# Kernel optimization log

Hardware: AMD Instinct MI355X
Metric: run time of the kernel (lower is better)

The kernel has to match this reference:

```python
import jax, jax.numpy as jnp
import numpy as np

B, S, E = 4, 2048, 768
DFF = 4 * E
EPS = 1e-5


def _layernorm(x, g, b):
    mu = jnp.mean(x, axis=-1, keepdims=True)
    var = jnp.mean(jnp.square(x - mu), axis=-1, keepdims=True)
    return (x - mu) * jax.lax.rsqrt(var + EPS) * g + b


def setup_inputs() -> dict:
    key = jax.random.key(0)
    ks = jax.random.split(key, 16)
    w = lambda k, shp: jax.random.normal(k, shp, dtype=jnp.float32) * 0.02
    inp = {
        "x": jax.random.normal(ks[0], (B, S, E), dtype=jnp.float32),
        "kv": jax.random.normal(ks[1], (B, S, E), dtype=jnp.float32),
        "wq_w": w(ks[2], (E, E)), "wq_b": jnp.zeros((E,), jnp.float32),
        "wk_w": w(ks[3], (E, E)), "wk_b": jnp.zeros((E,), jnp.float32),
        "wv_w": w(ks[4], (E, E)), "wv_b": jnp.zeros((E,), jnp.float32),
        "ln1_g": jnp.ones((E,), jnp.float32), "ln1_b": jnp.zeros((E,), jnp.float32),
        "wq2_w": w(ks[5], (E, E)), "wq2_b": jnp.zeros((E,), jnp.float32),
        "wk2_w": w(ks[6], (E, E)), "wk2_b": jnp.zeros((E,), jnp.float32),
        "wv2_w": w(ks[7], (E, E)), "wv2_b": jnp.zeros((E,), jnp.float32),
        "ln2_g": jnp.ones((E,), jnp.float32), "ln2_b": jnp.zeros((E,), jnp.float32),
        "w1": w(ks[8], (DFF, E)), "b1": jnp.zeros((DFF,), jnp.float32),
        "w2": w(ks[9], (E, DFF)), "b2": jnp.zeros((E,), jnp.float32),
        "ln3_g": jnp.ones((E,), jnp.float32), "ln3_b": jnp.zeros((E,), jnp.float32),
    }
    return inp


def reference(x, kv, wq_w, wq_b, wk_w, wk_b, wv_w, wv_b, ln1_g, ln1_b,
              wq2_w, wq2_b, wk2_w, wk2_b, wv2_w, wv2_b, ln2_g, ln2_b,
              w1, b1, w2, b2, ln3_g, ln3_b):
    scalar = 1.0 / np.sqrt(E).astype(np.float32)
    mask_value = jnp.finfo(x.dtype).min
    s = x.shape[1]
    causal = jnp.triu(jnp.ones((s, s), dtype=bool), k=1)  # True above diagonal -> masked

    # ---- causal self-attention (single head, full E) ----
    q = x @ wq_w.T + wq_b
    k = x @ wk_w.T + wk_b
    v = x @ wv_w.T + wv_b
    scores = jnp.einsum('bqe,bke->bqk', q, k) * scalar
    scores = jnp.where(causal, mask_value, scores)
    h1 = jnp.einsum('bqk,bke->bqe', jax.nn.softmax(scores, axis=-1), v)
    x = _layernorm(x + h1, ln1_g, ln1_b)

    # ---- cross-attention over kv (no mask) ----
    q2 = x @ wq2_w.T + wq2_b
    k2 = kv @ wk2_w.T + wk2_b
    v2 = kv @ wv2_w.T + wv2_b
    scores2 = jnp.einsum('bqe,bke->bqk', q2, k2) * scalar
    h2 = jnp.einsum('bqk,bke->bqe', jax.nn.softmax(scores2, axis=-1), v2)
    x = _layernorm(x + h2, ln2_g, ln2_b)

    # ---- MLP: Linear -> ReLU -> Linear -> ReLU (note trailing ReLU) ----
    h = jax.nn.relu(x @ w1.T + b1)
    mlp = jax.nn.relu(h @ w2.T + b2)
    return _layernorm(x + mlp, ln3_g, ln3_b)
```

## Files before the change

### kernel.cpp

```cpp
#include <hip/hip_runtime.h>
#include <hip/hip_bf16.h>
#include <math.h>


typedef __bf16 bf16_t;
typedef bf16_t bf16x8 __attribute__((ext_vector_type(8)));
typedef float f32x4 __attribute__((ext_vector_type(4)));

#define TBM 128
#define TBN 128
#define TBK 32
#define CPAD 136

struct MMDesc {
    const bf16_t* A;
    const bf16_t* B;
    const float* bias;
    __hip_bfloat16* C;
    float* lsum;
    int koff;
    int trans;
};
struct MMArgs { MMDesc g[8]; };

__device__ __forceinline__ void load16(const bf16_t* g, bf16_t* l) {
    __builtin_amdgcn_global_load_lds(
        (const __attribute__((address_space(1))) unsigned int*)g,
        (__attribute__((address_space(3))) unsigned int*)l, 16, 0, 0);
}

__device__ __forceinline__ void mm_core(
    const bf16_t* Ag, const bf16_t* Bg, int lda, int ldb, int K,
    bf16_t* Asm, bf16_t* Bsm, int w, int l, int wm, int wn, f32x4 acc[4][4]) {
    const int fr = l & 15;
    const int kq = (l >> 4) * 8;
    const long rsA = (long)64 * lda, rsB = (long)64 * ldb;
    bf16_t* Al = Asm + w * 512;
    bf16_t* Bl = Bsm + w * 512;

    for (int k0 = 0; k0 < K; k0 += 64) {
        load16(Ag + k0, Al);
        load16(Ag + rsA + k0, Al + 2048);
        load16(Bg + k0, Bl);
        load16(Bg + rsB + k0, Bl + 2048);
        load16(Ag + k0 + 32, Al + 4096);
        load16(Ag + rsA + k0 + 32, Al + 6144);
        load16(Bg + k0 + 32, Bl + 4096);
        load16(Bg + rsB + k0 + 32, Bl + 6144);
        __syncthreads();

#pragma unroll
        for (int t = 0; t < 2; ++t) {
            const bf16_t* As = Asm + t * 4096;
            const bf16_t* Bs = Bsm + t * 4096;
            bf16x8 af[4], bfr[4];
#pragma unroll
            for (int i = 0; i < 4; ++i)
                af[i] = *(const bf16x8*)(As + (wm + i * 16 + fr) * TBK + kq);
#pragma unroll
            for (int j = 0; j < 4; ++j)
                bfr[j] = *(const bf16x8*)(Bs + (wn + j * 16 + fr) * TBK + kq);
#pragma unroll
            for (int i = 0; i < 4; ++i)
#pragma unroll
                for (int j = 0; j < 4; ++j)
                    acc[i][j] = __builtin_amdgcn_mfma_f32_16x16x32_bf16(
                        af[i], bfr[j], acc[i][j], 0, 0, 0);
        }
        __syncthreads();
    }
}

__device__ __forceinline__ void tile_out(
    const __hip_bfloat16* ct, __hip_bfloat16* base, long ldc, int tid) {
#pragma unroll
    for (int u = 0; u < 8; ++u) {
        const int e = u * 2048 + tid * 8;
        const int rl = e >> 7, cl = e & 127;
        *(uint4*)(base + (long)rl * ldc + cl) = *(const uint4*)(ct + rl * CPAD + cl);
    }
}

template <bool RELU, bool CLAMPK>
__global__ __launch_bounds__(256) void mm_std(
    MMArgs args, int M, int N, int K, int lda, int ldb, float scale, int GX) {
    __shared__ __align__(16) bf16_t smem[128 * CPAD];
    bf16_t* Asm = smem;
    bf16_t* Bsm = smem + 8192;

    const MMDesc dsc = args.g[blockIdx.z];

    const int lin = blockIdx.x;
    const int panel = lin / (8 * GX);
    const int rem = lin - panel * 8 * GX;
    const int bx = rem >> 3;
    const int by = panel * 8 + (rem & 7);

    const int m0 = by * TBM, n0 = bx * TBN;
    const int tid = threadIdx.x, w = tid >> 6, l = tid & 63;
    const int wm = (w >> 1) * 64, wn = (w & 1) * 64;
    const int srow = w * 16 + (l >> 2);
    const int scol = (l & 3) * 8;
    const int fr = l & 15;

    f32x4 acc[4][4];
    const f32x4 z4 = {0.f, 0.f, 0.f, 0.f};
#pragma unroll
    for (int i = 0; i < 4; ++i)
#pragma unroll
        for (int j = 0; j < 4; ++j) acc[i][j] = z4;

    int Keff = K;
    if (CLAMPK) {
        int km = (by + 1) * TBM - dsc.koff;
        Keff = km < K ? km : K;
    }
    if (!CLAMPK || Keff > 0)
        mm_core(dsc.A + (long)(m0 + srow) * lda + scol,
                dsc.B + (long)(n0 + srow) * ldb + scol,
                lda, ldb, Keff, Asm, Bsm, w, l, wm, wn, acc);

    __hip_bfloat16* ct = (__hip_bfloat16*)smem;
    const int erow = (l >> 4) * 4;
#pragma unroll
    for (int j = 0; j < 4; ++j) {
        const int cl = wn + j * 16 + fr;
        const float bv = dsc.bias ? dsc.bias[n0 + cl] : 0.f;
#pragma unroll
        for (int i = 0; i < 4; ++i) {
            const int rl = wm + i * 16 + erow;
#pragma unroll
            for (int r = 0; r < 4; ++r) {
                float v = acc[i][j][r] * scale + bv;
                if (RELU) v = fmaxf(v, 0.f);
                const int idx = dsc.trans ? (cl * CPAD + rl + r) : ((rl + r) * CPAD + cl);
                ct[idx] = __float2bfloat16(v);
            }
        }
    }
    __syncthreads();
    __hip_bfloat16* base;
    long ldc;
    if (dsc.trans) {
        base = dsc.C + ((long)(m0 >> 11) * N + n0) * 2048 + (m0 & 2047);
        ldc = 2048;
    } else {
        base = dsc.C + (long)m0 * N + n0;
        ldc = N;
    }
    tile_out(ct, base, ldc, tid);
}

template <bool CAUSAL>
__global__ __launch_bounds__(256) void mm_exp(
    MMArgs args, int N, int K, int lda, int ldb, float scale, int GX) {
    __shared__ __align__(16) bf16_t smem[128 * CPAD];
    bf16_t* Asm = smem;
    bf16_t* Bsm = smem + 8192;

    const MMDesc dsc = args.g[blockIdx.z];

    int bx, by;
    if (CAUSAL) {
        const int t = blockIdx.x;
        by = (int)((sqrtf(8.f * t + 1.f) - 1.f) * 0.5f);
        while ((by + 1) * (by + 2) / 2 <= t) ++by;
        while (by * (by + 1) / 2 > t) --by;
        bx = t - by * (by + 1) / 2;
    } else {
        const int lin = blockIdx.x;
        const int panel = lin / (8 * GX);
        const int rem = lin - panel * 8 * GX;
        bx = rem >> 3;
        by = panel * 8 + (rem & 7);
    }

    const int m0 = by * TBM, n0 = bx * TBN;
    const int tid = threadIdx.x, w = tid >> 6, l = tid & 63;
    const int wm = (w >> 1) * 64, wn = (w & 1) * 64;
    const int srow = w * 16 + (l >> 2);
    const int scol = (l & 3) * 8;
    const int fr = l & 15;

    f32x4 acc[4][4];
    const f32x4 z4 = {0.f, 0.f, 0.f, 0.f};
#pragma unroll
    for (int i = 0; i < 4; ++i)
#pragma unroll
        for (int j = 0; j < 4; ++j) acc[i][j] = z4;

    mm_core(dsc.A + (long)(m0 + srow) * lda + scol,
            dsc.B + (long)(n0 + srow) * ldb + scol,
            lda, ldb, K, Asm, Bsm, w, l, wm, wn, acc);

    __hip_bfloat16* ct = (__hip_bfloat16*)smem;
    const int erow = (l >> 4) * 4;
#pragma unroll
    for (int i = 0; i < 4; ++i) {
#pragma unroll
        for (int r = 0; r < 4; ++r) {
            const int rl = wm + i * 16 + erow + r;
            const int grow = m0 + rl;
            float rs = 0.f;
#pragma unroll
            for (int j = 0; j < 4; ++j) {
                const int cl = wn + j * 16 + fr;
                float e;
                if (CAUSAL && (n0 + cl) > grow)
                    e = 0.f;
                else
                    e = __expf(acc[i][j][r] * scale);
                ct[rl * CPAD + cl] = __float2bfloat16(e);
                rs += e;
            }
#pragma unroll
            for (int o = 8; o > 0; o >>= 1) rs += __shfl_down(rs, o, 16);
            if ((l & 15) == 0) atomicAdd(&dsc.lsum[grow], rs);
        }
    }
    __syncthreads();
    tile_out(ct, dsc.C + (long)m0 * N + n0, N, tid);
}

__device__ __forceinline__ float waveReduceSum(float v) {
#pragma unroll
    for (int o = 32; o > 0; o >>= 1) v += __shfl_down(v, o, 64);
    return v;
}
__device__ __forceinline__ float blockReduceSum(float v, float* s) {
    int lane = threadIdx.x & 63, w = threadIdx.x >> 6;
    v = waveReduceSum(v);
    __syncthreads();
    if (lane == 0) s[w] = v;
    __syncthreads();
    return s[0] + s[1] + s[2] + s[3];
}

template <bool BR, bool XF32>
__global__ __launch_bounds__(256) void ln_kernel(
    const float* __restrict__ xf, const __hip_bfloat16* __restrict__ xh,
    const __hip_bfloat16* __restrict__ h1, const __hip_bfloat16* __restrict__ h2,
    const float* __restrict__ hbias, const float* __restrict__ lsum,
    const float* __restrict__ g, const float* __restrict__ beta,
    float* __restrict__ outf, __hip_bfloat16* __restrict__ outb) {
    __shared__ float red[4];
    const int E = 768;
    const long row = blockIdx.x;
    const float hscale = lsum ? (1.f / lsum[row]) : 1.f;

    float vals[3];
    float sum = 0.f;
#pragma unroll
    for (int i = 0; i < 3; ++i) {
        int c = threadIdx.x + i * 256;
        float t = __bfloat162float(h1[row * E + c]) + __bfloat162float(h2[row * E + c]);
        if (BR) t = fmaxf(t + hbias[c], 0.f);
        else t *= hscale;
        float xv = XF32 ? xf[row * E + c] : __bfloat162float(xh[row * E + c]);
        vals[i] = xv + t;
        sum += vals[i];
    }
    sum = blockReduceSum(sum, red);
    const float mean = sum * (1.f / 768.f);

    float ss = 0.f;
#pragma unroll
    for (int i = 0; i < 3; ++i) {
        float d = vals[i] - mean;
        ss += d * d;
    }
    ss = blockReduceSum(ss, red);
    const float inv = rsqrtf(ss * (1.f / 768.f) + 1e-5f);

#pragma unroll
    for (int i = 0; i < 3; ++i) {
        int c = threadIdx.x + i * 256;
        float v = (vals[i] - mean) * inv * g[c] + beta[c];
        if (outf) outf[row * E + c] = v;
        if (outb) outb[row * E + c] = __float2bfloat16(v);
    }
}

struct CvtPtrs {
    const float* s[10];
    __hip_bfloat16* d[10];
};
__global__ __launch_bounds__(256) void cvt_all(CvtPtrs p) {
    int bid = blockIdx.x, seg, off;
    if (bid < 3456) {
        seg = bid / 576;
        off = (bid % 576) * 1024;
    } else if (bid < 8064) {
        int t = bid - 3456;
        seg = 6 + t / 2304;
        off = (t % 2304) * 1024;
    } else {
        int t = bid - 8064;
        seg = 8 + t / 6144;
        off = (t % 6144) * 1024;
    }
    const float* s = p.s[seg];
    __hip_bfloat16* d = p.d[seg];
    int i = off + threadIdx.x * 4;
    float4 v = *(const float4*)(s + i);
    d[i + 0] = __float2bfloat16(v.x);
    d[i + 1] = __float2bfloat16(v.y);
    d[i + 2] = __float2bfloat16(v.z);
    d[i + 3] = __float2bfloat16(v.w);
}

extern "C" void kernel_launch(void* const* d_in, const int* in_sizes, int n_in,
                              void* d_out, int out_size, void* d_ws, size_t ws_size,
                              hipStream_t stream) {
    const int Bb = 4, S = 2048, E = 768, DFF = 3072;
    const int Nr = Bb * S;

    const float* x    = (const float*)d_in[0];
    const float* kv   = (const float*)d_in[1];
    const float* wq_w = (const float*)d_in[2];
    const float* wq_b = (const float*)d_in[3];
    const float* wk_w = (const float*)d_in[4];
    const float* wk_b = (const float*)d_in[5];
    const float* wv_w = (const float*)d_in[6];
    const float* wv_b = (const float*)d_in[7];
    const float* ln1g = (const float*)d_in[8];
    const float* ln1b = (const float*)d_in[9];
    const float* wq2w = (const float*)d_in[10];
    const float* wq2b = (const float*)d_in[11];
    const float* wk2w = (const float*)d_in[12];
    const float* wk2b = (const float*)d_in[13];
    const float* wv2w = (const float*)d_in[14];
    const float* wv2b = (const float*)d_in[15];
    const float* ln2g = (const float*)d_in[16];
    const float* ln2b = (const float*)d_in[17];
    const float* w1   = (const float*)d_in[18];
    const float* b1   = (const float*)d_in[19];
    const float* w2   = (const float*)d_in[20];
    const float* b2   = (const float*)d_in[21];
    const float* ln3g = (const float*)d_in[22];
    const float* ln3b = (const float*)d_in[23];
    float* out = (float*)d_out;

    char* wsp = (char*)d_ws;
    auto alloc = [&](size_t bytes) {
        char* p = wsp;
        wsp += (bytes + 255) & ~(size_t)255;
        return p;
    };
    const size_t nSE = (size_t)Nr * E;
    const size_t nSS = (size_t)Bb * S * S;
    __hip_bfloat16* Pb   = (__hip_bfloat16*)alloc(nSS * 2);
    __hip_bfloat16* qb   = (__hip_bfloat16*)alloc(nSE * 2);
    __hip_bfloat16* kb   = (__hip_bfloat16*)alloc(nSE * 2);
    __hip_bfloat16* hffb = Pb;
    __hip_bfloat16* vtb  = (__hip_bfloat16*)alloc(nSE * 2);
    __hip_bfloat16* xb   = (__hip_bfloat16*)alloc(nSE * 2);
    __hip_bfloat16* kvb  = (__hip_bfloat16*)alloc(nSE * 2);
    __hip_bfloat16* actb = (__hip_bfloat16*)alloc(nSE * 2);
    __hip_bfloat16* hA   = (__hip_bfloat16*)alloc(nSE * 2);
    __hip_bfloat16* hB   = (__hip_bfloat16*)alloc(nSE * 2);
    __hip_bfloat16* wqb   = (__hip_bfloat16*)alloc((size_t)E * E * 2);
    __hip_bfloat16* wkb   = (__hip_bfloat16*)alloc((size_t)E * E * 2);
    __hip_bfloat16* wvb   = (__hip_bfloat16*)alloc((size_t)E * E * 2);
    __hip_bfloat16* wq2bm = (__hip_bfloat16*)alloc((size_t)E * E * 2);
    __hip_bfloat16* wk2bm = (__hip_bfloat16*)alloc((size_t)E * E * 2);
    __hip_bfloat16* wv2bm = (__hip_bfloat16*)alloc((size_t)E * E * 2);
    __hip_bfloat16* w1b   = (__hip_bfloat16*)alloc((size_t)DFF * E * 2);
    __hip_bfloat16* w2b   = (__hip_bfloat16*)alloc((size_t)E * DFF * 2);
    float* lsum1 = (float*)alloc((size_t)Nr * 4);
    float* lsum2 = (float*)alloc((size_t)Nr * 4);

    const float scale = 1.0f / sqrtf((float)E);
    const dim3 blk(256);

    hipMemsetAsync(lsum1, 0, (size_t)Nr * 4 * 2, stream);

    CvtPtrs cp;
    cp.s[0] = wq_w; cp.d[0] = wqb;
    cp.s[1] = wk_w; cp.d[1] = wkb;
    cp.s[2] = wv_w; cp.d[2] = wvb;
    cp.s[3] = wq2w; cp.d[3] = wq2bm;
    cp.s[4] = wk2w; cp.d[4] = wk2bm;
    cp.s[5] = wv2w; cp.d[5] = wv2bm;
    cp.s[6] = w1;   cp.d[6] = w1b;
    cp.s[7] = w2;   cp.d[7] = w2b;
    cp.s[8] = x;    cp.d[8] = xb;
    cp.s[9] = kv;   cp.d[9] = kvb;
    cvt_all<<<8064 + 12288, blk, 0, stream>>>(cp);

    {
        MMArgs a{};
        a.g[0] = {(const bf16_t*)xb, (const bf16_t*)wqb, wq_b, qb, nullptr, 0, 0};
        a.g[1] = {(const bf16_t*)xb, (const bf16_t*)wkb, wk_b, kb, nullptr, 0, 0};
        a.g[2] = {(const bf16_t*)xb, (const bf16_t*)wvb, wv_b, vtb, nullptr, 0, 1};
        mm_std<false, false><<<dim3(6 * 64, 1, 3), blk, 0, stream>>>(
            a, Nr, E, E, E, E, 1.f, 6);
    }
    {
        MMArgs a{};
        for (int b = 0; b < 4; ++b)
            a.g[b] = {(const bf16_t*)qb + (long)b * S * E,
                      (const bf16_t*)kb + (long)b * S * E, nullptr,
                      Pb + (long)b * S * S, lsum1 + b * S, 0, 0};
        mm_exp<true><<<dim3(136, 1, 4), blk, 0, stream>>>(a, S, E, E, E, scale, 16);
    }
    {
        MMArgs a{};
        for (int b = 0; b < 4; ++b)
            for (int ks = 0; ks < 2; ++ks)
                a.g[b * 2 + ks] = {(const bf16_t*)Pb + (long)b * S * S + ks * 1024,
                                   (const bf16_t*)vtb + (long)b * E * S + ks * 1024,
                                   nullptr, (ks ? hB : hA) + (long)b * S * E,
                                   nullptr, ks * 1024, 0};
        mm_std<false, true><<<dim3(6 * 16, 1, 8), blk, 0, stream>>>(
            a, S, E, 1024, S, S, 1.f, 6);
    }
    ln_kernel<false, true><<<Nr, blk, 0, stream>>>(
        x, nullptr, hA, hB, nullptr, lsum1, ln1g, ln1b, nullptr, actb);

    {
        MMArgs a{};
        a.g[0] = {(const bf16_t*)actb, (const bf16_t*)wq2bm, wq2b, qb, nullptr, 0, 0};
        a.g[1] = {(const bf16_t*)kvb, (const bf16_t*)wk2bm, wk2b, kb, nullptr, 0, 0};
        a.g[2] = {(const bf16_t*)kvb, (const bf16_t*)wv2bm, wv2b, vtb, nullptr, 0, 1};
        mm_std<false, false><<<dim3(6 * 64, 1, 3), blk, 0, stream>>>(
            a, Nr, E, E, E, E, 1.f, 6);
    }
    {
        MMArgs a{};
        for (int b = 0; b < 4; ++b)
            a.g[b] = {(const bf16_t*)qb + (long)b * S * E,
                      (const bf16_t*)kb + (long)b * S * E, nullptr,
                      Pb + (long)b * S * S, lsum2 + b * S, 0, 0};
        mm_exp<false><<<dim3(16 * 16, 1, 4), blk, 0, stream>>>(a, S, E, E, E, scale, 16);
    }
    {
        MMArgs a{};
        for (int b = 0; b < 4; ++b)
            for (int ks = 0; ks < 2; ++ks)
                a.g[b * 2 + ks] = {(const bf16_t*)Pb + (long)b * S * S + ks * 1024,
                                   (const bf16_t*)vtb + (long)b * E * S + ks * 1024,
                                   nullptr, (ks ? hB : hA) + (long)b * S * E,
                                   nullptr, 0, 0};
        mm_std<false, false><<<dim3(6 * 16, 1, 8), blk, 0, stream>>>(
            a, S, E, 1024, S, S, 1.f, 6);
    }
    ln_kernel<false, false><<<Nr, blk, 0, stream>>>(
        nullptr, actb, hA, hB, nullptr, lsum2, ln2g, ln2b, nullptr, actb);

    {
        MMArgs a{};
        a.g[0] = {(const bf16_t*)actb, (const bf16_t*)w1b, b1, hffb, nullptr, 0, 0};
        mm_std<true, false><<<dim3(24 * 64, 1, 1), blk, 0, stream>>>(
            a, Nr, DFF, E, E, E, 1.f, 24);
    }
    {
        MMArgs a{};
        a.g[0] = {(const bf16_t*)hffb, (const bf16_t*)w2b, nullptr, hA, nullptr, 0, 0};
        a.g[1] = {(const bf16_t*)hffb + 1536, (const bf16_t*)w2b + 1536, nullptr,
                  hB, nullptr, 0, 0};
        mm_std<false, false><<<dim3(6 * 64, 1, 2), blk, 0, stream>>>(
            a, Nr, E, 1536, DFF, DFF, 1.f, 6);
    }
    ln_kernel<true, false><<<Nr, blk, 0, stream>>>(
        nullptr, actb, hA, hB, b2, nullptr, ln3g, ln3b, out, nullptr);
}
```

Measured before the change: 561.2 us.

## Replace GEMM core with 256x256 tile, 8-wave ping-pong pipelined MFMA kernel

Replaces the 128x128, 4-wave GEMM core with a 256x256 tile kernel run by 512 threads. It double-buffers K-tiles in 128KB of LDS using an XOR-swizzled layout, and interleaves global-to-LDS loads with MFMA phases through explicit barriers, waitcnts and s_setprio. The aim is higher arithmetic intensity per block and loads that overlap compute, removing the load-then-sync stalls of the old loop. The risks are fewer blocks on small GEMMs (fewer than the CU count in some launches), coarser causal tile skipping, and fragile hand-scheduled synchronisation that assumes K is a multiple of 128.

```diff
diff --git a/kernel.cpp b/kernel.cpp
--- a/kernel.cpp
+++ b/kernel.cpp
@@ -6,11 +6,6 @@
 typedef __bf16 bf16_t;
 typedef bf16_t bf16x8 __attribute__((ext_vector_type(8)));
 typedef float f32x4 __attribute__((ext_vector_type(4)));
-
-#define TBM 128
-#define TBN 128
-#define TBK 32
-#define CPAD 136
 
 struct MMDesc {
     const bf16_t* A;
@@ -29,65 +24,109 @@
         (__attribute__((address_space(3))) unsigned int*)l, 16, 0, 0);
 }
 
-__device__ __forceinline__ void mm_core(
+__device__ __forceinline__ void rd4(const bf16_t* p, int s0, int s1, bf16x8 f[4][2]) {
+#pragma unroll
+    for (int i = 0; i < 4; ++i) {
+        f[i][0] = *(const bf16x8*)(p + i * 1024 + s0);
+        f[i][1] = *(const bf16x8*)(p + i * 1024 + s1);
+    }
+}
+__device__ __forceinline__ void rd2(const bf16_t* p, int s0, int s1, bf16x8 f[2][2]) {
+#pragma unroll
+    for (int i = 0; i < 2; ++i) {
+        f[i][0] = *(const bf16x8*)(p + i * 1024 + s0);
+        f[i][1] = *(const bf16x8*)(p + i * 1024 + s1);
+    }
+}
+
+#define SBAR asm volatile("s_barrier" ::: "memory")
+#define SCH  __builtin_amdgcn_sched_barrier(0)
+#define MID  do { SCH; SBAR; SCH; __builtin_amdgcn_s_setprio(1); } while (0)
+#define END0 do { __builtin_amdgcn_s_setprio(0); SCH; \
+    asm volatile("s_waitcnt lgkmcnt(0)" ::: "memory"); SBAR; SCH; } while (0)
+#define ENDV do { __builtin_amdgcn_s_setprio(0); SCH; \
+    asm volatile("s_waitcnt vmcnt(4) lgkmcnt(0)" ::: "memory"); SBAR; SCH; } while (0)
+
+#define QMFMA(mh, nh, BF) do { \
+    _Pragma("unroll") \
+    for (int ks = 0; ks < 2; ++ks) \
+    _Pragma("unroll") \
+    for (int mi = 0; mi < 4; ++mi) \
+    _Pragma("unroll") \
+    for (int ni = 0; ni < 2; ++ni) \
+        acc[(mh) * 4 + mi][(nh) * 2 + ni] = __builtin_amdgcn_mfma_f32_16x16x32_bf16( \
+            af[mi][ks], BF[ni][ks], acc[(mh) * 4 + mi][(nh) * 2 + ni], 0, 0, 0); \
+} while (0)
+
+__device__ __forceinline__ void mm8_core(
     const bf16_t* Ag, const bf16_t* Bg, int lda, int ldb, int K,
-    bf16_t* Asm, bf16_t* Bsm, int w, int l, int wm, int wn, f32x4 acc[4][4]) {
-    const int fr = l & 15;
-    const int kq = (l >> 4) * 8;
-    const long rsA = (long)64 * lda, rsB = (long)64 * ldb;
-    bf16_t* Al = Asm + w * 512;
-    bf16_t* Bl = Bsm + w * 512;
-
-    for (int k0 = 0; k0 < K; k0 += 64) {
-        load16(Ag + k0, Al);
-        load16(Ag + rsA + k0, Al + 2048);
-        load16(Bg + k0, Bl);
-        load16(Bg + rsB + k0, Bl + 2048);
-        load16(Ag + k0 + 32, Al + 4096);
-        load16(Ag + rsA + k0 + 32, Al + 6144);
-        load16(Bg + k0 + 32, Bl + 4096);
-        load16(Bg + rsB + k0 + 32, Bl + 6144);
-        __syncthreads();
-
-#pragma unroll
-        for (int t = 0; t < 2; ++t) {
-            const bf16_t* As = Asm + t * 4096;
-            const bf16_t* Bs = Bsm + t * 4096;
-            bf16x8 af[4], bfr[4];
-#pragma unroll
-            for (int i = 0; i < 4; ++i)
-                af[i] = *(const bf16x8*)(As + (wm + i * 16 + fr) * TBK + kq);
-#pragma unroll
-            for (int j = 0; j < 4; ++j)
-                bfr[j] = *(const bf16x8*)(Bs + (wn + j * 16 + fr) * TBK + kq);
-#pragma unroll
-            for (int i = 0; i < 4; ++i)
-#pragma unroll
-                for (int j = 0; j < 4; ++j)
-                    acc[i][j] = __builtin_amdgcn_mfma_f32_16x16x32_bf16(
-                        af[i], bfr[j], acc[i][j], 0, 0, 0);
-        }
-        __syncthreads();
-    }
-}
-
-__device__ __forceinline__ void tile_out(
-    const __hip_bfloat16* ct, __hip_bfloat16* base, long ldc, int tid) {
-#pragma unroll
-    for (int u = 0; u < 8; ++u) {
-        const int e = u * 2048 + tid * 8;
-        const int rl = e >> 7, cl = e & 127;
-        *(uint4*)(base + (long)rl * ldc + cl) = *(const uint4*)(ct + rl * CPAD + cl);
-    }
+    bf16_t* lds, int w, int l, f32x4 acc[8][4])
+{
+    const long ldal = lda, ldbl = ldb;
+    const int fr = l & 15, kq = l >> 4;
+    const int rr = w * 8 + (l >> 3);
+    const int c8e = ((l & 7) ^ (l >> 3)) * 8;
+    const bf16_t* As = Ag + (long)rr * ldal + c8e;
+    const bf16_t* Bs = Bg + (long)rr * ldbl + c8e;
+    const int s0 = ((0 + kq) ^ (fr & 7)) * 8;
+    const int s1 = ((4 + kq) ^ (fr & 7)) * 8;
+    const bf16_t* lA = lds + ((w >> 2) * 64 + fr) * 64;
+    const bf16_t* lB = lds + 16384 + ((w & 3) * 32 + fr) * 64;
+    bf16_t* stA = lds + w * 512;
+    bf16_t* stB = lds + 16384 + w * 512;
+
+    auto stg = [&](int b, int isB, int h, int t) {
+        const long ld = isB ? ldbl : ldal;
+        const bf16_t* g = (isB ? Bs : As) + (long)h * 128 * ld + (long)t * 64;
+        bf16_t* d = (isB ? stB : stA) + b * 32768 + h * 8192;
+        load16(g, d);
+        load16(g + 64 * ld, d + 4096);
+    };
+
+    bf16x8 af[4][2], bf0[2][2], bf1[2][2];
+    const int NT = K >> 6, NI = NT >> 1;
+
+    stg(0, 0, 0, 0); stg(0, 1, 0, 0); stg(0, 1, 1, 0); stg(0, 0, 1, 0);
+    stg(1, 0, 0, 1); stg(1, 1, 0, 1);
+    asm volatile("s_waitcnt vmcnt(4)" ::: "memory");
+    SBAR; SCH;
+
+    for (int i = 0; i < NI; ++i) {
+        const int t1 = 2 * i + 1;
+        int t2 = 2 * i + 2; if (t2 >= NT) t2 -= 2;
+        int t3 = 2 * i + 3; if (t3 >= NT) t3 -= 2;
+        rd4(lA, s0, s1, af); rd2(lB, s0, s1, bf0);
+        stg(1, 1, 1, t1);
+        MID; QMFMA(0, 0, bf0); END0;
+        rd2(lB + 8192, s0, s1, bf1);
+        stg(1, 0, 1, t1);
+        MID; QMFMA(0, 1, bf1); END0;
+        rd4(lA + 8192, s0, s1, af);
+        stg(0, 0, 0, t2);
+        MID; QMFMA(1, 0, bf0); END0;
+        stg(0, 1, 0, t2);
+        MID; QMFMA(1, 1, bf1); ENDV;
+        rd4(lA + 32768, s0, s1, af); rd2(lB + 32768, s0, s1, bf0);
+        stg(0, 1, 1, t2);
+        MID; QMFMA(0, 0, bf0); END0;
+        rd2(lB + 32768 + 8192, s0, s1, bf1);
+        stg(0, 0, 1, t2);
+        MID; QMFMA(0, 1, bf1); END0;
+        rd4(lA + 32768 + 8192, s0, s1, af);
+        stg(1, 0, 0, t3);
+        MID; QMFMA(1, 0, bf0); END0;
+        stg(1, 1, 0, t3);
+        MID; QMFMA(1, 1, bf1); ENDV;
+    }
+    asm volatile("s_waitcnt vmcnt(0)" ::: "memory");
+    SBAR; SCH;
 }
 
 template <bool RELU, bool CLAMPK>
-__global__ __launch_bounds__(256) void mm_std(
-    MMArgs args, int M, int N, int K, int lda, int ldb, float scale, int GX) {
-    __shared__ __align__(16) bf16_t smem[128 * CPAD];
-    bf16_t* Asm = smem;
-    bf16_t* Bsm = smem + 8192;
-
+__global__ __launch_bounds__(512, 2) void mm8_std(
+    MMArgs args, int M, int N, int K, int lda, int ldb, float scale, int GX)
+{
+    __shared__ __align__(16) bf16_t lds[65536];
     const MMDesc dsc = args.g[blockIdx.z];
 
     const int lin = blockIdx.x;
@@ -95,69 +134,77 @@
     const int rem = lin - panel * 8 * GX;
     const int bx = rem >> 3;
     const int by = panel * 8 + (rem & 7);
-
-    const int m0 = by * TBM, n0 = bx * TBN;
+    const int m0 = by * 256, n0 = bx * 256;
     const int tid = threadIdx.x, w = tid >> 6, l = tid & 63;
-    const int wm = (w >> 1) * 64, wn = (w & 1) * 64;
-    const int srow = w * 16 + (l >> 2);
-    const int scol = (l & 3) * 8;
-    const int fr = l & 15;
-
-    f32x4 acc[4][4];
+
+    f32x4 acc[8][4];
     const f32x4 z4 = {0.f, 0.f, 0.f, 0.f};
 #pragma unroll
-    for (int i = 0; i < 4; ++i)
+    for (int i = 0; i < 8; ++i)
 #pragma unroll
         for (int j = 0; j < 4; ++j) acc[i][j] = z4;
 
     int Keff = K;
     if (CLAMPK) {
-        int km = (by + 1) * TBM - dsc.koff;
+        int km = (by + 1) * 256 - dsc.koff;
         Keff = km < K ? km : K;
     }
     if (!CLAMPK || Keff > 0)
-        mm_core(dsc.A + (long)(m0 + srow) * lda + scol,
-                dsc.B + (long)(n0 + srow) * ldb + scol,
-                lda, ldb, Keff, Asm, Bsm, w, l, wm, wn, acc);
-
-    __hip_bfloat16* ct = (__hip_bfloat16*)smem;
-    const int erow = (l >> 4) * 4;
-#pragma unroll
-    for (int j = 0; j < 4; ++j) {
-        const int cl = wn + j * 16 + fr;
-        const float bv = dsc.bias ? dsc.bias[n0 + cl] : 0.f;
-#pragma unroll
-        for (int i = 0; i < 4; ++i) {
-            const int rl = wm + i * 16 + erow;
-#pragma unroll
-            for (int r = 0; r < 4; ++r) {
-                float v = acc[i][j][r] * scale + bv;
-                if (RELU) v = fmaxf(v, 0.f);
-                const int idx = dsc.trans ? (cl * CPAD + rl + r) : ((rl + r) * CPAD + cl);
-                ct[idx] = __float2bfloat16(v);
+        mm8_core(dsc.A + (long)m0 * lda, dsc.B + (long)n0 * ldb,
+                 lda, ldb, Keff, lds, w, l, acc);
+
+    const int fr = l & 15, erow = (l >> 4) * 4;
+    const int wrow = (w >> 2) * 64, wcol = (w & 3) * 32;
+    __hip_bfloat16* ct = (__hip_bfloat16*)lds;
+#pragma unroll
+    for (int mh = 0; mh < 2; ++mh) {
+        if (mh) __syncthreads();
+#pragma unroll
+        for (int nh = 0; nh < 2; ++nh)
+#pragma unroll
+            for (int ni = 0; ni < 2; ++ni) {
+                const int cl = nh * 128 + wcol + ni * 16 + fr;
+                const float bv = dsc.bias ? dsc.bias[n0 + cl] : 0.f;
+#pragma unroll
+                for (int mi = 0; mi < 4; ++mi) {
+                    const int lr = wrow + mi * 16 + erow;
+                    const f32x4 a = acc[mh * 4 + mi][nh * 2 + ni];
+#pragma unroll
+                    for (int r = 0; r < 4; ++r) {
+                        float v = a[r] * scale + bv;
+                        if (RELU) v = fmaxf(v, 0.f);
+                        ct[dsc.trans ? (cl * 136 + lr + r) : ((lr + r) * 264 + cl)]
+                            = __float2bfloat16(v);
+                    }
+                }
+            }
+        __syncthreads();
+        if (dsc.trans) {
+            __hip_bfloat16* base = dsc.C + ((long)(m0 >> 11) * N + n0) * 2048
+                                 + (m0 & 2047) + mh * 128;
+#pragma unroll
+            for (int u = 0; u < 8; ++u) {
+                const int e = u * 4096 + tid * 8;
+                *(uint4*)(base + (long)(e >> 7) * 2048 + (e & 127))
+                    = *(const uint4*)(ct + (e >> 7) * 136 + (e & 127));
+            }
+        } else {
+            __hip_bfloat16* base = dsc.C + (long)(m0 + mh * 128) * N + n0;
+#pragma unroll
+            for (int u = 0; u < 8; ++u) {
+                const int e = u * 4096 + tid * 8;
+                *(uint4*)(base + (long)(e >> 8) * N + (e & 255))
+                    = *(const uint4*)(ct + (e >> 8) * 264 + (e & 255));
             }
         }
     }
-    __syncthreads();
-    __hip_bfloat16* base;
-    long ldc;
-    if (dsc.trans) {
-        base = dsc.C + ((long)(m0 >> 11) * N + n0) * 2048 + (m0 & 2047);
-        ldc = 2048;
-    } else {
-        base = dsc.C + (long)m0 * N + n0;
-        ldc = N;
-    }
-    tile_out(ct, base, ldc, tid);
 }
 
 template <bool CAUSAL>
-__global__ __launch_bounds__(256) void mm_exp(
-    MMArgs args, int N, int K, int lda, int ldb, float scale, int GX) {
-    __shared__ __align__(16) bf16_t smem[128 * CPAD];
-    bf16_t* Asm = smem;
-    bf16_t* Bsm = smem + 8192;
-
+__global__ __launch_bounds__(512, 2) void mm8_exp(
+    MMArgs args, int N, int K, int lda, int ldb, float scale, int GX)
+{
+    __shared__ __align__(16) bf16_t lds[65536];
     const MMDesc dsc = args.g[blockIdx.z];
 
     int bx, by;
@@ -174,52 +221,59 @@
         bx = rem >> 3;
         by = panel * 8 + (rem & 7);
     }
-
-    const int m0 = by * TBM, n0 = bx * TBN;
+    const int m0 = by * 256, n0 = bx * 256;
     const int tid = threadIdx.x, w = tid >> 6, l = tid & 63;
-    const int wm = (w >> 1) * 64, wn = (w & 1) * 64;
-    const int srow = w * 16 + (l >> 2);
-    const int scol = (l & 3) * 8;
-    const int fr = l & 15;
-
-    f32x4 acc[4][4];
+
+    f32x4 acc[8][4];
     const f32x4 z4 = {0.f, 0.f, 0.f, 0.f};
 #pragma unroll
-    for (int i = 0; i < 4; ++i)
+    for (int i = 0; i < 8; ++i)
 #pragma unroll
         for (int j = 0; j < 4; ++j) acc[i][j] = z4;
 
-    mm_core(dsc.A + (long)(m0 + srow) * lda + scol,
-            dsc.B + (long)(n0 + srow) * ldb + scol,
-            lda, ldb, K, Asm, Bsm, w, l, wm, wn, acc);
-
-    __hip_bfloat16* ct = (__hip_bfloat16*)smem;
-    const int erow = (l >> 4) * 4;
-#pragma unroll
-    for (int i = 0; i < 4; ++i) {
-#pragma unroll
-        for (int r = 0; r < 4; ++r) {
-            const int rl = wm + i * 16 + erow + r;
-            const int grow = m0 + rl;
-            float rs = 0.f;
-#pragma unroll
-            for (int j = 0; j < 4; ++j) {
-                const int cl = wn + j * 16 + fr;
-                float e;
-                if (CAUSAL && (n0 + cl) > grow)
-                    e = 0.f;
-                else
-                    e = __expf(acc[i][j][r] * scale);
-                ct[rl * CPAD + cl] = __float2bfloat16(e);
-                rs += e;
+    mm8_core(dsc.A + (long)m0 * lda, dsc.B + (long)n0 * ldb,
+             lda, ldb, K, lds, w, l, acc);
+
+    const int fr = l & 15, erow = (l >> 4) * 4;
+    const int wrow = (w >> 2) * 64, wcol = (w & 3) * 32;
+    __hip_bfloat16* ct = (__hip_bfloat16*)lds;
+#pragma unroll
+    for (int mh = 0; mh < 2; ++mh) {
+        if (mh) __syncthreads();
+#pragma unroll
+        for (int mi = 0; mi < 4; ++mi) {
+            const int lr = wrow + mi * 16 + erow;
+#pragma unroll
+            for (int r = 0; r < 4; ++r) {
+                const int grow = m0 + mh * 128 + lr + r;
+                float rs = 0.f;
+#pragma unroll
+                for (int nh = 0; nh < 2; ++nh)
+#pragma unroll
+                    for (int ni = 0; ni < 2; ++ni) {
+                        const int cl = nh * 128 + wcol + ni * 16 + fr;
+                        float e;
+                        if (CAUSAL && (n0 + cl) > grow)
+                            e = 0.f;
+                        else
+                            e = __expf(acc[mh * 4 + mi][nh * 2 + ni][r] * scale);
+                        ct[(lr + r) * 264 + cl] = __float2bfloat16(e);
+                        rs += e;
+                    }
+#pragma unroll
+                for (int o = 8; o > 0; o >>= 1) rs += __shfl_down(rs, o, 16);
+                if ((l & 15) == 0) atomicAdd(&dsc.lsum[grow], rs);
             }
-#pragma unroll
-            for (int o = 8; o > 0; o >>= 1) rs += __shfl_down(rs, o, 16);
-            if ((l & 15) == 0) atomicAdd(&dsc.lsum[grow], rs);
         }
-    }
-    __syncthreads();
-    tile_out(ct, dsc.C + (long)m0 * N + n0, N, tid);
+        __syncthreads();
+        __hip_bfloat16* base = dsc.C + (long)(m0 + mh * 128) * N + n0;
+#pragma unroll
+        for (int u = 0; u < 8; ++u) {
+            const int e = u * 4096 + tid * 8;
+            *(uint4*)(base + (long)(e >> 8) * N + (e & 255))
+                = *(const uint4*)(ct + (e >> 8) * 264 + (e & 255));
+        }
+    }
 }
 
 __device__ __forceinline__ float waveReduceSum(float v) {
@@ -372,6 +426,7 @@
 
     const float scale = 1.0f / sqrtf((float)E);
     const dim3 blk(256);
+    const dim3 blk5(512);
 
     hipMemsetAsync(lsum1, 0, (size_t)Nr * 4 * 2, stream);
 
@@ -393,8 +448,8 @@
         a.g[0] = {(const bf16_t*)xb, (const bf16_t*)wqb, wq_b, qb, nullptr, 0, 0};
         a.g[1] = {(const bf16_t*)xb, (const bf16_t*)wkb, wk_b, kb, nullptr, 0, 0};
         a.g[2] = {(const bf16_t*)xb, (const bf16_t*)wvb, wv_b, vtb, nullptr, 0, 1};
-        mm_std<false, false><<<dim3(6 * 64, 1, 3), blk, 0, stream>>>(
-            a, Nr, E, E, E, E, 1.f, 6);
+        mm8_std<false, false><<<dim3(96, 1, 3), blk5, 0, stream>>>(
+            a, Nr, E, E, E, E, 1.f, 3);
     }
     {
         MMArgs a{};
@@ -402,7 +457,7 @@
             a.g[b] = {(const bf16_t*)qb + (long)b * S * E,
                       (const bf16_t*)kb + (long)b * S * E, nullptr,
                       Pb + (long)b * S * S, lsum1 + b * S, 0, 0};
-        mm_exp<true><<<dim3(136, 1, 4), blk, 0, stream>>>(a, S, E, E, E, scale, 16);
+        mm8_exp<true><<<dim3(36, 1, 4), blk5, 0, stream>>>(a, S, E, E, E, scale, 8);
     }
     {
         MMArgs a{};
@@ -412,8 +467,8 @@
                                    (const bf16_t*)vtb + (long)b * E * S + ks * 1024,
                                    nullptr, (ks ? hB : hA) + (long)b * S * E,
                                    nullptr, ks * 1024, 0};
-        mm_std<false, true><<<dim3(6 * 16, 1, 8), blk, 0, stream>>>(
-            a, S, E, 1024, S, S, 1.f, 6);
+        mm8_std<false, true><<<dim3(24, 1, 8), blk5, 0, stream>>>(
+            a, S, E, 1024, S, S, 1.f, 3);
     }
     ln_kernel<false, true><<<Nr, blk, 0, stream>>>(
         x, nullptr, hA, hB, nullptr, lsum1, ln1g, ln1b, nullptr, actb);
@@ -423,8 +478,8 @@
         a.g[0] = {(const bf16_t*)actb, (const bf16_t*)wq2bm, wq2b, qb, nullptr, 0, 0};
         a.g[1] = {(const bf16_t*)kvb, (const bf16_t*)wk2bm, wk2b, kb, nullptr, 0, 0};
         a.g[2] = {(const bf16_t*)kvb, (const bf16_t*)wv2bm, wv2b, vtb, nullptr, 0, 1};
-        mm_std<false, false><<<dim3(6 * 64, 1, 3), blk, 0, stream>>>(
-            a, Nr, E, E, E, E, 1.f, 6);
+        mm8_std<false, false><<<dim3(96, 1, 3), blk5, 0, stream>>>(
+            a, Nr, E, E, E, E, 1.f, 3);
     }
     {
         MMArgs a{};
@@ -432,7 +487,7 @@
             a.g[b] = {(const bf16_t*)qb + (long)b * S * E,
                       (const bf16_t*)kb + (long)b * S * E, nullptr,
                       Pb + (long)b * S * S, lsum2 + b * S, 0, 0};
-        mm_exp<false><<<dim3(16 * 16, 1, 4), blk, 0, stream>>>(a, S, E, E, E, scale, 16);
+        mm8_exp<false><<<dim3(64, 1, 4), blk5, 0, stream>>>(a, S, E, E, E, scale, 8);
     }
     {
         MMArgs a{};
@@ -442,8 +497,8 @@
                                    (const bf16_t*)vtb + (long)b * E * S + ks * 1024,
                                    nullptr, (ks ? hB : hA) + (long)b * S * E,
                                    nullptr, 0, 0};
-        mm_std<false, false><<<dim3(6 * 16, 1, 8), blk, 0, stream>>>(
-            a, S, E, 1024, S, S, 1.f, 6);
+        mm8_std<false, false><<<dim3(24, 1, 8), blk5, 0, stream>>>(
+            a, S, E, 1024, S, S, 1.f, 3);
     }
     ln_kernel<false, false><<<Nr, blk, 0, stream>>>(
         nullptr, actb, hA, hB, nullptr, lsum2, ln2g, ln2b, nullptr, actb);
@@ -451,16 +506,16 @@
     {
         MMArgs a{};
         a.g[0] = {(const bf16_t*)actb, (const bf16_t*)w1b, b1, hffb, nullptr, 0, 0};
-        mm_std<true, false><<<dim3(24 * 64, 1, 1), blk, 0, stream>>>(
-            a, Nr, DFF, E, E, E, 1.f, 24);
+        mm8_std<true, false><<<dim3(384, 1, 1), blk5, 0, stream>>>(
+            a, Nr, DFF, E, E, E, 1.f, 12);
     }
     {
         MMArgs a{};
         a.g[0] = {(const bf16_t*)hffb, (const bf16_t*)w2b, nullptr, hA, nullptr, 0, 0};
         a.g[1] = {(const bf16_t*)hffb + 1536, (const bf16_t*)w2b + 1536, nullptr,
                   hB, nullptr, 0, 0};
-        mm_std<false, false><<<dim3(6 * 64, 1, 2), blk, 0, stream>>>(
-            a, Nr, E, 1536, DFF, DFF, 1.f, 6);
+        mm8_std<false, false><<<dim3(96, 1, 2), blk5, 0, stream>>>(
+            a, Nr, E, 1536, DFF, DFF, 1.f, 3);
     }
     ln_kernel<true, false><<<Nr, blk, 0, stream>>>(
         nullptr, actb, hA, hB, b2, nullptr, ln3g, ln3b, out, nullptr);
```

Measured after the change: 542.7 us. -3.3%, faster.
